# Kernel optimization log

Hardware: AMD Instinct MI355X
Metric: run time of the kernel (lower is better)

## Reference

```python
import jax, jax.numpy as jnp
import numpy as np

EMB = 300; H = 150; DEC = 300
VU = 50000; VQ = 30000; VS = 5000
N_COLS = 64; COL_LEN = 6; N_TURNS = 6; IN_LEN = 128; GEN_LEN = 64
MAX_KEEP = 5


def _lstm_cell(x, h, c, Wih, Whh, b):
    z = x @ Wih.T + h @ Whh.T + b
    i, f, g, o = jnp.split(z, 4)
    c = jax.nn.sigmoid(f) * c + jax.nn.sigmoid(i) * jnp.tanh(g)
    h = jax.nn.sigmoid(o) * jnp.tanh(c)
    return h, c


def _run_lstm(xs, Wih, Whh, b):
    hsz = Whh.shape[-1]
    z = jnp.zeros((hsz,), xs.dtype)
    def step(carry, x):
        h, c = _lstm_cell(x, carry[0], carry[1], Wih, Whh, b)
        return (h, c), h
    (h, c), ys = jax.lax.scan(step, (z, z), xs)
    return ys, h, c


def _bilstm(xs, Wih, Whh, b):
    # Wih: [2, 4H, in], Whh: [2, 4H, H], b: [2, 4H]
    yf, hf, cf = _run_lstm(xs, Wih[0], Whh[0], b[0])
    yb, hb, cb = _run_lstm(xs[::-1], Wih[1], Whh[1], b[1])
    return jnp.concatenate([yf, yb[::-1]], -1), jnp.concatenate([hf, hb], -1), jnp.concatenate([cf, cb], -1)


def _attention(q, keys, Wq, Wk, v):
    # Bahdanau: v^T tanh(Wq q + Wk k); context = softmax-weighted sum of keys
    s = jnp.tanh(q @ Wq + keys @ Wk) @ v
    return jax.nn.softmax(s) @ keys


def _forward(utter_emb, query_emb, schema_tok_emb, enc_Wih, enc_Whh, enc_b,
             attn_Wq, attn_Wk, attn_v, dec_Wih0, dec_Whh0, dec_b0,
             dec_Wih1, dec_Whh1, dec_b1, transform_W, sql_W, sql_b, col_W,
             schema_tokens, input_seqs, output_gt):
    attn = lambda k_i, q, keys: _attention(q, keys, attn_Wq[k_i], attn_Wk[k_i], attn_v[k_i])
    # --- schema column encoding: BiLSTM over each column's name tokens ---
    col_tok = schema_tok_emb[schema_tokens]                       # [C, L, EMB]
    _, h, _ = jax.vmap(lambda xs: _bilstm(xs, enc_Wih[0], enc_Whh[0], enc_b[0]))(col_tok)
    schema_embs = h                                               # [C, EMB]
    prev_in, prev_h, prev_c, prev_out = [], [], [], []
    all_dists = []
    bos_emb = query_emb[0]
    for i in range(N_TURNS):
        idx = input_seqs[i]
        # mixed vocab / schema-pointer embedding lookup
        x = jnp.where((idx < VU)[:, None],
                      utter_emb[jnp.clip(idx, 0, VU - 1)],
                      schema_embs[jnp.clip(idx - VU, 0, N_COLS - 1)])
        x, _, _ = _bilstm(x, enc_Wih[1], enc_Whh[1], enc_b[1])    # utter_encoder
        # TextSchemaEncoder (approx): second BiLSTM + schema cross-attention update
        x, fh, fc = _bilstm(x, enc_Wih[2], enc_Whh[2], enc_b[2])
        schema_embs = schema_embs + jax.nn.softmax(schema_embs @ x.T, -1) @ x
        h0, c0 = fh, fc
        if i > 0:
            hist_h = jnp.stack(prev_h); hist_c = jnp.stack(prev_c)
            h0n = h0 + attn(0, h0, hist_h)
            c0 = h0n + attn(0, c0, hist_c)  # replicates original's h-based c init
            h0 = h0n
        prev_in = (prev_in + [x])[:MAX_KEEP]
        prev_h = (prev_h + [fh])[:MAX_KEEP]
        prev_c = (prev_c + [fc])[:MAX_KEEP]
        keys_in = jnp.concatenate(prev_in, 0)
        keys_out = jnp.concatenate(prev_out, 0) if i > 0 else None
        se = schema_embs

        def embed_out(t):
            return jnp.where(t < VQ,
                             query_emb[jnp.clip(t, 0, VQ - 1)],
                             se[jnp.clip(t - VQ, 0, N_COLS - 1)])

        def dec_step(carry, t):
            h1p, c1p, h2p, c2p, dh = carry
            out_emb = embed_out(t)  # teacher forcing
            ctx_s = attn(1, dh, se)
            ctx_i = attn(2, dh, keys_in)
            ctx_o = attn(3, dh, keys_out) if keys_out is not None else jnp.zeros_like(ctx_i)
            ctx = jnp.concatenate([ctx_s, ctx_i, ctx_o])
            xin = jnp.concatenate([out_emb, ctx])                 # [4*EMB]
            h1, c1 = _lstm_cell(xin, h1p, c1p, dec_Wih0, dec_Whh0, dec_b0)
            h2, c2 = _lstm_cell(h1, h2p, c2p, dec_Wih1, dec_Whh1, dec_b1)
            out = jnp.tanh(jnp.concatenate([h2, ctx]) @ transform_W.T)
            score = jnp.concatenate([out @ sql_W.T + sql_b, (out @ col_W.T) @ se.T])
            dist = jax.nn.log_softmax(score)
            am_emb = embed_out(jnp.argmax(dist))
            return (h1, c1, h2, c2, h2), (dist, am_emb)

        init = (h0, c0, h0, c0, h0)
        _, (dists, am_embs) = jax.lax.scan(dec_step, init, output_gt[i, :GEN_LEN - 1])
        prev_out = (prev_out + [jnp.concatenate([bos_emb[None], am_embs], 0)])[:MAX_KEEP]
        all_dists.append(dists)
    return jnp.stack(all_dists, 0)  # [N_TURNS, GEN_LEN-1, VQ+N_COLS]


def setup_inputs() -> dict:
    key = jax.random.key(0)
    ks = jax.random.split(key, 24)
    s = 0.05
    f = lambda k, shape: jax.random.normal(k, shape, jnp.float32) * s
    return {
        "utter_emb": f(ks[0], (VU, EMB)),
        "query_emb": f(ks[1], (VQ, EMB)),
        "schema_tok_emb": f(ks[2], (VS, EMB)),
        "enc_Wih": f(ks[3], (3, 2, 4 * H, EMB)),   # [schema, utter, text-schema] x [fwd, bwd]
        "enc_Whh": f(ks[4], (3, 2, 4 * H, H)),
        "enc_b": f(ks[5], (3, 2, 4 * H)),
        "attn_Wq": f(ks[6], (4, EMB, EMB)),        # [turn, schema, in_tok, out_tok]
        "attn_Wk": f(ks[7], (4, EMB, EMB)),
        "attn_v": f(ks[8], (4, EMB)),
        "dec_Wih0": f(ks[9], (4 * DEC, 4 * EMB)),
        "dec_Whh0": f(ks[10], (4 * DEC, DEC)),
        "dec_b0": f(ks[11], (4 * DEC,)),
        "dec_Wih1": f(ks[12], (4 * DEC, DEC)),
        "dec_Whh1": f(ks[13], (4 * DEC, DEC)),
        "dec_b1": f(ks[14], (4 * DEC,)),
        "transform_W": f(ks[15], (EMB, 4 * EMB)),
        "sql_W": f(ks[16], (VQ, EMB)),
        "sql_b": f(ks[17], (VQ,)),
        "col_W": f(ks[18], (EMB, EMB)),
        "schema_tokens": jax.random.randint(ks[19], (N_COLS, COL_LEN), 0, VS),
        "input_seqs": jax.random.randint(ks[20], (N_TURNS, IN_LEN), 0, VU + N_COLS),
        "output_gt": jax.random.randint(ks[21], (N_TURNS, GEN_LEN), 0, VQ + N_COLS),
    }


def reference(utter_emb, query_emb, schema_tok_emb, enc_Wih, enc_Whh, enc_b,
              attn_Wq, attn_Wk, attn_v, dec_Wih0, dec_Whh0, dec_b0,
              dec_Wih1, dec_Whh1, dec_b1, transform_W, sql_W, sql_b, col_W,
              schema_tokens, input_seqs, output_gt):
    return _forward(utter_emb, query_emb, schema_tok_emb, enc_Wih, enc_Whh, enc_b,
                    attn_Wq, attn_Wk, attn_v, dec_Wih0, dec_Whh0, dec_b0,
                    dec_Wih1, dec_Whh1, dec_b1, transform_W, sql_W, sql_b, col_W,
                    schema_tokens, input_seqs, output_gt)
```

## Files before the change

kernel.cpp:

```cpp
#include <hip/hip_runtime.h>

#define EMB 300
#define VU 50000
#define VQ 30000
#define NCOLS 64
#define COLLEN 6
#define NTURNS 6
#define INLEN 128
#define TSTEPS 63
#define VOUT 30064
#define MAXK 5
#define NWD 60
#define FPAD 32
#define SENTU 0x7FC00001u

__device__ __forceinline__ float sigf(float x){ return 1.0f/(1.0f+__expf(-x)); }
__device__ __forceinline__ float tanhf_(float x){ return 1.0f - 2.0f/(1.0f+__expf(2.0f*x)); }
__device__ __forceinline__ float wsum(float v){
#pragma unroll
  for (int o=32;o;o>>=1) v += __shfl_xor(v,o);
  return v;
}
__device__ __forceinline__ float wmax(float v){
#pragma unroll
  for (int o=32;o;o>>=1) v = fmaxf(v,__shfl_xor(v,o));
  return v;
}

__device__ __forceinline__ void gstore(float* p, float v){
  __hip_atomic_store((int*)p, __float_as_int(v), __ATOMIC_RELAXED, __HIP_MEMORY_SCOPE_AGENT);
}
__device__ __forceinline__ float gload(const float* p){
  return __int_as_float(__hip_atomic_load((const int*)p, __ATOMIC_RELAXED, __HIP_MEMORY_SCOPE_AGENT));
}

__device__ __forceinline__ void garrive(int* flags, int w, int P){
  asm volatile("s_waitcnt vmcnt(0)" ::: "memory");
  __syncthreads();
  if (threadIdx.x == 0)
    __hip_atomic_store(flags + w*FPAD, P, __ATOMIC_RELAXED, __HIP_MEMORY_SCOPE_AGENT);
}
__device__ __forceinline__ void gwait(const int* flags, int P){
  if (threadIdx.x < 64) {
    int v;
    do {
      v = (threadIdx.x < NWD) ? __hip_atomic_load(flags + threadIdx.x*FPAD, __ATOMIC_RELAXED, __HIP_MEMORY_SCOPE_AGENT) : P;
    } while (__any(v < P));
  }
  __syncthreads();
}

template<int MAXV>
__device__ __forceinline__ void pollfetch(const float* __restrict__ src, float* dstLDS,
                                          int n, int modstride, int tid, volatile int* okf)
{
  float v[MAXV]; bool val[MAXV]; int idx[MAXV];
#pragma unroll
  for (int k = 0; k < MAXV; ++k) {
    idx[k] = tid + 256*k;
    bool ib = idx[k] < n;
    if (modstride) {
      int m = idx[k];
      while (m >= modstride) m -= modstride;
      ib = ib && (m < 300);
    }
    val[k] = ib;
  }
  for (;;) {
    bool ok = true;
#pragma unroll
    for (int k = 0; k < MAXV; ++k)
      if (val[k]) { v[k] = gload(src + idx[k]); ok = ok && (__float_as_uint(v[k]) != SENTU); }
    if (!__all(ok) && (tid & 63) == 0) *okf = 0;
    __syncthreads();
    int done = *okf;
    __syncthreads();
    if (done) break;
    if (tid == 0) *okf = 1;
    __syncthreads();
  }
#pragma unroll
  for (int k = 0; k < MAXV; ++k) if (val[k]) dstLDS[idx[k]] = v[k];
  __syncthreads();
}

__global__ void k_init(int* flags){
  for (int i = threadIdx.x; i < NWD*FPAD; i += 256) flags[i] = 0;
}

__global__ void k_transposeB(const float* __restrict__ in, float* __restrict__ out,
                             int R, int C, size_t mstride)
{
  __shared__ float tile[32][33];
  const float* inp = in + (size_t)blockIdx.z*mstride;
  float* outp = out + (size_t)blockIdx.z*mstride;
  const int rb = blockIdx.y*32, cb = blockIdx.x*32;
  const int tx = threadIdx.x & 31, ty = threadIdx.x >> 5;
  for (int k = 0; k < 32; k += 8) {
    int r = rb + ty + k, c = cb + tx;
    if (r < R && c < C) tile[ty+k][tx] = inp[(size_t)r*C + c];
  }
  __syncthreads();
  for (int k = 0; k < 32; k += 8) {
    int c = cb + ty + k, r = rb + tx;
    if (c < C && r < R) outp[(size_t)c*R + r] = tile[tx][ty+k];
  }
}

__global__ void k_schema(const float* __restrict__ temb, const int* __restrict__ stok,
                         const float* __restrict__ Wih, const float* __restrict__ Whh,
                         const float* __restrict__ bb, float* __restrict__ SE0)
{
  const int col = blockIdx.x >> 1, dir = blockIdx.x & 1, tid = threadIdx.x;
  __shared__ float hl[150], cl[150], zl[600];
  if (tid < 150) { hl[tid]=0.f; cl[tid]=0.f; }
  __syncthreads();
  const float* Wi = Wih + (size_t)dir*600*300;
  const float* Wh = Whh + (size_t)dir*600*150;
  const float* bd = bb + dir*600;
  for (int s = 0; s < COLLEN; ++s) {
    const int pos = dir ? (COLLEN-1-s) : s;
    const int tok = stok[col*COLLEN + pos];
    const float* x = temb + (size_t)tok*300;
    for (int g = tid; g < 600; g += 256) {
      float a = bd[g];
      const float* wi = Wi + (size_t)g*300;
      for (int c = 0; c < 300; ++c) a += x[c]*wi[c];
      const float* wh = Wh + (size_t)g*150;
      for (int j = 0; j < 150; ++j) a += hl[j]*wh[j];
      zl[g] = a;
    }
    __syncthreads();
    if (tid < 150) {
      float ii=zl[tid], ff=zl[150+tid], gg=zl[300+tid], oo=zl[450+tid];
      float cn = sigf(ff)*cl[tid] + sigf(ii)*tanhf_(gg);
      cl[tid]=cn; hl[tid]=sigf(oo)*tanhf_(cn);
    }
    __syncthreads();
  }
  if (tid < 150) SE0[(size_t)col*300 + dir*150 + tid] = hl[tid];
}

__global__ void k_gemm_xe(const float* __restrict__ src, const float* __restrict__ SEi,
                          const int* __restrict__ iseq, int mode,
                          const float* __restrict__ WihT, const float* __restrict__ bL,
                          float* __restrict__ Xg)
{
  const int g = blockIdx.x*256 + threadIdx.x;
  if (g >= 1200) return;
  const int p0 = blockIdx.y*16;
  const float* xr[16];
#pragma unroll
  for (int t = 0; t < 16; ++t) {
    int p = p0 + t;
    if (mode) xr[t] = src + (size_t)p*300;
    else {
      int tok = iseq[p];
      xr[t] = (tok < VU) ? src + (size_t)tok*300 : SEi + (size_t)(tok - VU)*300;
    }
  }
  const float b = bL[g];
  float acc[16];
#pragma unroll
  for (int t = 0; t < 16; ++t) acc[t] = b;
  for (int c = 0; c < 300; ++c) {
    float wv = WihT[(size_t)c*1200 + g];
#pragma unroll
    for (int t = 0; t < 16; ++t) acc[t] += wv * xr[t][c];
  }
#pragma unroll
  for (int t = 0; t < 16; ++t) Xg[(size_t)(p0+t)*1200 + g] = acc[t];
}

__global__ __launch_bounds__(640) void k_rec(
    const float* __restrict__ Xg, const float* __restrict__ WhhTL,
    float* __restrict__ ys, float* __restrict__ fh, float* __restrict__ fc)
{
  const int dir = blockIdx.x, tid = threadIdx.x;
  __shared__ __align__(16) float hl[152];
  __shared__ float cl[152], zl[600];
  float w[150];
  const float* wt = WhhTL + (size_t)dir*150*600;
  if (tid < 600) {
#pragma unroll
    for (int j = 0; j < 150; ++j) w[j] = wt[(size_t)j*600 + tid];
  }
  if (tid < 152) { hl[tid] = 0.f; cl[tid] = 0.f; }
  __syncthreads();
  float xg = (tid < 600) ? Xg[(size_t)(dir ? INLEN-1 : 0)*1200 + dir*600 + tid] : 0.f;
  for (int s = 0; s < INLEN; ++s) {
    const int pos = dir ? (INLEN-1-s) : s;
    const int nxt = dir ? (INLEN-2-s) : (s+1);
    float xg_nx = (s+1 < INLEN && tid < 600) ? Xg[(size_t)nxt*1200 + dir*600 + tid] : 0.f;
    if (tid < 600) {
      float aa[8];
#pragma unroll
      for (int q = 0; q < 8; ++q) aa[q] = 0.f;
      const float4* h4 = (const float4*)hl;
#pragma unroll
      for (int j4 = 0; j4 < 37; ++j4) {
        float4 h = h4[j4];
        aa[j4&7] += w[4*j4]*h.x + w[4*j4+1]*h.y + w[4*j4+2]*h.z + w[4*j4+3]*h.w;
      }
      zl[tid] = xg + ((aa[0]+aa[1])+(aa[2]+aa[3])) + ((aa[4]+aa[5])+(aa[6]+aa[7]))
                + w[148]*hl[148] + w[149]*hl[149];
    }
    __syncthreads();
    if (tid < 150) {
      float ii=zl[tid], ff=zl[150+tid], gg=zl[300+tid], oo=zl[450+tid];
      float cn = sigf(ff)*cl[tid] + sigf(ii)*tanhf_(gg);
      cl[tid] = cn;
      float hn = sigf(oo)*tanhf_(cn);
      hl[tid] = hn;
      ys[(size_t)pos*300 + dir*150 + tid] = hn;
    }
    __syncthreads();
    xg = xg_nx;
  }
  if (tid < 150) { fh[dir*150 + tid] = hl[tid]; fc[dir*150 + tid] = cl[tid]; }
}

__global__ void k_schema_upd(const float* __restrict__ SEi, const float* __restrict__ ys2,
                             float* __restrict__ SEo,
                             const float* __restrict__ fh, const float* __restrict__ fc,
                             float* __restrict__ HH, float* __restrict__ CH,
                             float* __restrict__ XH, int turn)
{
  const int row = blockIdx.x, tid = threadIdx.x;
  __shared__ float sl[300], al[128], red[4];
  for (int d = tid; d < 300; d += 256) sl[d] = SEi[(size_t)row*300 + d];
  __syncthreads();
  if (tid < 128) {
    float a = 0;
    const float* yr = ys2 + (size_t)tid*300;
    for (int d = 0; d < 300; ++d) a += sl[d]*yr[d];
    al[tid] = a;
  }
  __syncthreads();
  if (tid < 64) { float m = fmaxf(al[tid], al[tid+64]); m = wmax(m); if (tid==0) red[0]=m; }
  __syncthreads();
  if (tid < 128) al[tid] = __expf(al[tid] - red[0]);
  __syncthreads();
  if (tid < 64) { float s = al[tid] + al[tid+64]; s = wsum(s); if (tid==0) red[1]=s; }
  __syncthreads();
  const float invz = 1.0f/red[1];
  for (int d = tid; d < 300; d += 256) {
    float a = sl[d];
    for (int j = 0; j < 128; ++j) a += (al[j]*invz) * ys2[(size_t)j*300 + d];
    SEo[(size_t)row*300 + d] = a;
  }
  if (turn < MAXK) {
    for (int i = row*600 + tid; i < row*600 + 600; i += 256)
      XH[(size_t)turn*INLEN*300 + i] = ys2[i];
    if (row == 0)
      for (int d = tid; d < 300; d += 256) { HH[turn*300+d] = fh[d]; CH[turn*300+d] = fc[d]; }
  }
}

__device__ __forceinline__ const float* key_ptr(int j, int nin, const float* SE1,
                                                const float* XH, const float* OH, int* fam)
{
  if (j < 64) { *fam = 0; return SE1 + (size_t)j*300; }
  if (j < 64+nin) { *fam = 1; return XH + (size_t)(j-64)*300; }
  *fam = 2; return OH + (size_t)(j-64-nin)*300;
}

__global__ __launch_bounds__(256) void k_g1k(
    const float* __restrict__ SE1, const float* __restrict__ XH,
    const float* __restrict__ OH, const float* __restrict__ Wih0,
    float* __restrict__ G1KT, int nin, int nout)
{
  const int NK = 64 + nin + nout;
  const int tid = threadIdx.x;
  const int j0 = blockIdx.x*32, r0 = blockIdx.y*64;
  __shared__ float A[32][301];
  int fam; const float* base = key_ptr(j0, nin, SE1, XH, OH, &fam);
  const int wv = tid >> 6, ln = tid & 63;
  for (int jj = wv*8; jj < wv*8+8; ++jj)
    for (int c = ln; c < 300; c += 64)
      A[jj][c] = base[(size_t)jj*300 + c];
  __syncthreads();
  const int j = tid & 31, rb = tid >> 5;
  const int cb = 300 + fam*300;
  float acc[8] = {0,0,0,0,0,0,0,0};
  const float* Wp[8]; bool vld[8];
#pragma unroll
  for (int i = 0; i < 8; ++i) {
    int r = r0 + rb + 8*i;
    vld[i] = (r < 1200);
    Wp[i] = Wih0 + (size_t)(vld[i] ? r : 0)*1200 + cb;
  }
  for (int c = 0; c < 300; ++c) {
    float a = A[j][c];
#pragma unroll
    for (int i = 0; i < 8; ++i) acc[i] += a * Wp[i][c];
  }
#pragma unroll
  for (int i = 0; i < 8; ++i) {
    int r = r0 + rb + 8*i;
    if (vld[i]) G1KT[(size_t)r*NK + j0 + j] = acc[i];
  }
}

__global__ void k_tables(const float* __restrict__ SE1, const float* __restrict__ XH,
                         const float* __restrict__ OH, const float* __restrict__ Wk,
                         const float* __restrict__ Wih0T, const float* __restrict__ b0,
                         const float* __restrict__ tWT, const float* __restrict__ qemb,
                         const int* __restrict__ gt,
                         float* __restrict__ KW, float* __restrict__ G2K,
                         float* __restrict__ Ew, int nin, int nout)
{
  const int NK = 64 + nin + nout;
  const int b = blockIdx.x;
  if (b < NK) {
    int fam; const float* Kr = key_ptr(b, nin, SE1, XH, OH, &fam);
    const float* W = Wk + (size_t)(1+fam)*90000;
    for (int c = threadIdx.x; c < 300; c += 256) {
      float a = 0;
      for (int d = 0; d < 300; ++d) a += Kr[d]*W[(size_t)d*300 + c];
      KW[(size_t)b*300 + c] = a;
    }
  } else if (b < 2*NK) {
    int j = b - NK;
    int fam; const float* Kr = key_ptr(j, nin, SE1, XH, OH, &fam);
    const int cb = 300 + fam*300;
    for (int r = threadIdx.x; r < 300; r += 256) {
      float a = 0;
      for (int c = 0; c < 300; ++c) a += Kr[c]*tWT[(size_t)(cb+c)*300 + r];
      G2K[(size_t)j*300 + r] = a;
    }
  } else {
    int t = b - 2*NK;
    int tok = gt[t];
    const float* e = (tok < VQ) ? qemb + (size_t)tok*300 : SE1 + (size_t)(tok-VQ)*300;
    for (int r = threadIdx.x; r < 1200; r += 256) {
      float a = b0[r];
      for (int c = 0; c < 300; ++c) a += e[c]*Wih0T[(size_t)c*1200 + r];
      Ew[(size_t)t*1200 + r] = a;
    }
  }
}

__global__ __launch_bounds__(256, 1) void k_dec(
    const float* __restrict__ KW, const float* __restrict__ G1KT,
    const float* __restrict__ Ew, const float* __restrict__ WqT,
    const float* __restrict__ av, const float* __restrict__ Wq0,
    const float* __restrict__ Wk0,
    const float* __restrict__ Whh0, const float* __restrict__ Wih1,
    const float* __restrict__ Whh1, const float* __restrict__ b1,
    const float* __restrict__ fh, const float* __restrict__ fc,
    const float* __restrict__ HH, const float* __restrict__ CH,
    float* __restrict__ h0b, float* __restrict__ c0b,
    float* __restrict__ xQW, float* __restrict__ xSC,
    float* __restrict__ xH1, float* __restrict__ xH2,
    float* __restrict__ Alog, float* __restrict__ H2log,
    int nin, int nout, int turn, int* __restrict__ flags)
{
  const int NK = 64 + nin + nout;
  const int w = blockIdx.x, tid = threadIdx.x;
  const int wv = tid >> 6, ln = tid & 63;
  __shared__ float g1kl[20][1024];
  __shared__ float kwl[18][320];
  __shared__ float qWlp[3][320];
  __shared__ float vllp[3][320];
  __shared__ float ewl[63][20];
  __shared__ float scl[1024];
  __shared__ float dhl[320], h1l[320];
  __shared__ float pre1[20], pre2[20], zl[20], c1l[5], c2l[5];
  __shared__ float redA[4], alscA[8];
  __shared__ float wr0[4], wr1[4], wr2[4], rm[3], rz[3];
  __shared__ int okf;
  const float SENTF = __uint_as_float(SENTU);

  for (int i = w*256 + tid; i < TSTEPS*960;  i += NWD*256) gstore(xQW + i, SENTF);
  for (int i = w*256 + tid; i < TSTEPS*1024; i += NWD*256) gstore(xSC + i, SENTF);
  for (int i = w*256 + tid; i < TSTEPS*320;  i += NWD*256) gstore(xH1 + i, SENTF);
  for (int i = w*256 + tid; i < TSTEPS*320;  i += NWD*256) gstore(xH2 + i, SENTF);

  for (int i = tid; i < 20*1024; i += 256) {
    int o = i >> 10, j = i & 1023;
    int row = w*5 + (o % 5) + 300*(o / 5);
    g1kl[o][j] = (j < NK) ? G1KT[(size_t)row*NK + j] : 0.f;
  }
  for (int i = tid; i < 18*320; i += 256) {
    int jo = i / 320, c = i - jo*320;
    int j = w*18 + jo;
    kwl[jo][c] = (c < 300 && j < NK) ? KW[(size_t)j*300 + c] : 0.f;
  }
  for (int i = tid; i < 3*320; i += 256) {
    int f = i / 320, c = i - f*320;
    vllp[f][c] = (c < 300) ? av[300 + f*300 + c] : 0.f;
    qWlp[f][c] = 0.f;
  }
  for (int i = tid; i < 63*20; i += 256) {
    int t = i / 20, o = i - t*20;
    int row = w*5 + (o % 5) + 300*(o / 5);
    ewl[t][o] = Ew[(size_t)t*1200 + row];
  }
  if (tid < 20) { dhl[300+tid] = 0.f; h1l[300+tid] = 0.f; }
  if (tid == 0) okf = 1;

  float rwh0[5][5], rwh1[5][5], rwi1[5][5], rwq4[4][5], b1r[5];
#pragma unroll
  for (int r = 0; r < 5; ++r) {
    int row = w*5 + r + 300*wv;
    b1r[r] = b1[row];
#pragma unroll
    for (int k = 0; k < 5; ++k) {
      int d = ln + 64*k;
      rwh0[r][k] = (d < 300) ? Whh0[(size_t)row*300 + d] : 0.f;
      rwh1[r][k] = (d < 300) ? Whh1[(size_t)row*300 + d] : 0.f;
      rwi1[r][k] = (d < 300) ? Wih1[(size_t)row*300 + d] : 0.f;
    }
  }
#pragma unroll
  for (int r = 0; r < 4; ++r) {
    int o = r*4 + wv;
    int q = w*15 + ((o < 15) ? o : 0);
    int fam = q / 300, c = q - fam*300;
    const float* bp = WqT + ((size_t)(1+fam)*300 + c)*300;
#pragma unroll
    for (int k = 0; k < 5; ++k) {
      int d = ln + 64*k;
      rwq4[r][k] = (o < 15 && d < 300) ? bp[d] : 0.f;
    }
  }
  const int jlo = (w*18 < NK) ? w*18 : NK-1;
  const int jhi = (w*18+17 < NK) ? w*18+17 : NK-1;
  const int f0 = (jlo < 64) ? 0 : (jlo < 64+nin ? 1 : 2);
  const int f1 = (jhi < 64) ? 0 : (jhi < 64+nin ? 1 : 2);
  __syncthreads();

  if (w == 0) {
    if (turn == 0) {
      for (int d = tid; d < 300; d += 256) { gstore(h0b+d, fh[d]); gstore(c0b+d, fc[d]); }
    } else {
      const int nh = turn;
      for (int d = tid; d < 300; d += 256) dhl[d] = fh[d];
      __syncthreads();
      for (int rep = 0; rep < 2; ++rep) {
        const float* keys = rep ? CH : HH;
        for (int c = tid; c < 300; c += 256) {
          float a = 0;
          for (int d = 0; d < 300; ++d) a += dhl[d]*Wq0[(size_t)d*300 + c];
          h1l[c] = a;
        }
        __syncthreads();
        for (int k = 0; k < nh; ++k) {
          const float* Kr = keys + (size_t)k*300;
          float part = 0;
          for (int c = tid; c < 300; c += 256) {
            float kw = 0;
            for (int d = 0; d < 300; ++d) kw += Kr[d]*Wk0[(size_t)d*300 + c];
            part += av[c]*tanhf_(h1l[c] + kw);
          }
          part = wsum(part);
          if (ln == 0) redA[wv] = part;
          __syncthreads();
          if (tid == 0) alscA[k] = redA[0]+redA[1]+redA[2]+redA[3];
          __syncthreads();
        }
        if (tid == 0) {
          float m = -1e30f;
          for (int k = 0; k < nh; ++k) m = fmaxf(m, alscA[k]);
          float z = 0;
          for (int k = 0; k < nh; ++k) { alscA[k] = __expf(alscA[k]-m); z += alscA[k]; }
          for (int k = 0; k < nh; ++k) alscA[k] /= z;
        }
        __syncthreads();
        if (rep == 0) {
          for (int c = tid; c < 300; c += 256) {
            float a = dhl[c];
            for (int k = 0; k < nh; ++k) a += alscA[k]*keys[(size_t)k*300 + c];
            scl[c] = a; gstore(h0b+c, a);
          }
          __syncthreads();
          for (int d = tid; d < 300; d += 256) dhl[d] = fc[d];
          __syncthreads();
        } else {
          for (int c = tid; c < 300; c += 256) {
            float a = scl[c];
            for (int k = 0; k < nh; ++k) a += alscA[k]*keys[(size_t)k*300 + c];
            gstore(c0b+c, a);
          }
        }
      }
    }
  }
  garrive(flags, w, turn+1);
  gwait(flags, turn+1);

  for (int i = tid; i < 300; i += 256) { float v = gload(h0b+i); dhl[i] = v; h1l[i] = v; }
  if (tid < 5) { float v = gload(c0b + w*5 + tid); c1l[tid] = v; c2l[tid] = v; }
  __syncthreads();

  for (int t = 0; t < TSTEPS; ++t) {
    if (t) pollfetch<2>(xH2 + (size_t)(t-1)*320, dhl, 300, 0, tid, &okf);
#pragma unroll
    for (int r = 0; r < 4; ++r) {
      float a = 0;
#pragma unroll
      for (int k = 0; k < 5; ++k) a += rwq4[r][k]*dhl[ln + 64*k];
      a = wsum(a);
      int o = r*4 + wv;
      if (ln == 0 && o < 15) {
        int q = w*15 + o, fam = q/300, c = q - fam*300;
        gstore(xQW + (size_t)t*960 + fam*320 + c, a);
      }
    }
#pragma unroll
    for (int r = 0; r < 5; ++r) {
      float a1 = 0, a2 = 0;
#pragma unroll
      for (int k = 0; k < 5; ++k) {
        float hv = h1l[ln + 64*k], dv = dhl[ln + 64*k];
        a1 += rwh0[r][k]*hv; a2 += rwh1[r][k]*dv;
      }
      a1 = wsum(a1); a2 = wsum(a2);
      if (ln == 0) { pre1[wv*5+r] = a1; pre2[wv*5+r] = a2 + b1r[r]; }
    }

    pollfetch<3>(xQW + (size_t)t*960 + f0*320, &qWlp[f0][0], (f1-f0+1)*320, 320, tid, &okf);
#pragma unroll
    for (int r = 0; r < 5; ++r) {
      int jo = wv*5 + r;
      int j = w*18 + jo;
      bool va = (jo < 18) && (j < NK);
      int f = va ? ((j < 64) ? 0 : (j < 64+nin ? 1 : 2)) : 0;
      int jc = (jo < 18) ? jo : 0;
      float a = 0;
#pragma unroll
      for (int k = 0; k < 5; ++k) {
        int c = ln + 64*k;
        a += vllp[f][c] * tanhf_(qWlp[f][c] + kwl[jc][c]);
      }
      a = wsum(a);
      if (ln == 0 && va) gstore(xSC + (size_t)t*1024 + j, a);
    }

    pollfetch<4>(xSC + (size_t)t*1024, scl, NK, 0, tid, &okf);
    {
      float m0=-1e30f, m1=-1e30f, m2=-1e30f;
      for (int j = tid; j < NK; j += 256) {
        float x = scl[j];
        if (j < 64) m0 = fmaxf(m0,x); else if (j < 64+nin) m1 = fmaxf(m1,x); else m2 = fmaxf(m2,x);
      }
      m0 = wmax(m0); m1 = wmax(m1); m2 = wmax(m2);
      if (ln==0){ wr0[wv]=m0; wr1[wv]=m1; wr2[wv]=m2; }
      __syncthreads();
      if (tid==0){
        rm[0]=fmaxf(fmaxf(wr0[0],wr0[1]),fmaxf(wr0[2],wr0[3]));
        rm[1]=fmaxf(fmaxf(wr1[0],wr1[1]),fmaxf(wr1[2],wr1[3]));
        rm[2]=fmaxf(fmaxf(wr2[0],wr2[1]),fmaxf(wr2[2],wr2[3]));
      }
      __syncthreads();
      float s0=0,s1=0,s2=0;
      for (int j = tid; j < NK; j += 256) {
        int f = (j<64)?0:(j<64+nin?1:2);
        float e = __expf(scl[j] - rm[f]);
        scl[j] = e;
        if (f==0) s0+=e; else if (f==1) s1+=e; else s2+=e;
      }
      s0=wsum(s0); s1=wsum(s1); s2=wsum(s2);
      if (ln==0){ wr0[wv]=s0; wr1[wv]=s1; wr2[wv]=s2; }
      __syncthreads();
      if (tid==0){
        rz[0]=wr0[0]+wr0[1]+wr0[2]+wr0[3];
        rz[1]=wr1[0]+wr1[1]+wr1[2]+wr1[3];
        rz[2]=wr2[0]+wr2[1]+wr2[2]+wr2[3];
      }
      __syncthreads();
      for (int j = tid; j < NK; j += 256) {
        int f = (j<64)?0:(j<64+nin?1:2);
        scl[j] /= rz[f];
      }
      __syncthreads();
    }
    {
      const int KC = NK >> 6;
#pragma unroll 1
      for (int r = 0; r < 5; ++r) {
        int o = wv*5 + r;
        float a = 0;
        for (int k = 0; k < KC; ++k) { int j = ln + 64*k; a += scl[j]*g1kl[o][j]; }
        a = wsum(a);
        if (ln == 0) zl[o] = a + ewl[t][o] + pre1[o];
      }
    }
    __syncthreads();
    if (tid < 5) {
      float ii=zl[tid], ff=zl[5+tid], gg=zl[10+tid], oo=zl[15+tid];
      float cn = sigf(ff)*c1l[tid] + sigf(ii)*tanhf_(gg);
      c1l[tid] = cn;
      gstore(xH1 + (size_t)t*320 + w*5 + tid, sigf(oo)*tanhf_(cn));
    }
    if (tid < 18) { int j = w*18 + tid; if (j < NK) Alog[(size_t)t*1024 + j] = scl[j]; }

    pollfetch<2>(xH1 + (size_t)t*320, h1l, 300, 0, tid, &okf);
#pragma unroll
    for (int r = 0; r < 5; ++r) {
      float a = 0;
#pragma unroll
      for (int k = 0; k < 5; ++k) a += rwi1[r][k]*h1l[ln + 64*k];
      a = wsum(a);
      if (ln == 0) zl[wv*5+r] = a + pre2[wv*5+r];
    }
    __syncthreads();
    if (tid < 5) {
      int d = w*5 + tid;
      float ii=zl[tid], ff=zl[5+tid], gg=zl[10+tid], oo=zl[15+tid];
      float cn = sigf(ff)*c2l[tid] + sigf(ii)*tanhf_(gg);
      c2l[tid] = cn;
      float hn = sigf(oo)*tanhf_(cn);
      gstore(xH2 + (size_t)t*320 + d, hn);
      H2log[(size_t)t*300 + d] = hn;
    }
  }
}

__global__ void k_ctxout2(const float* __restrict__ H2, const float* __restrict__ Al,
                          const float* __restrict__ G2K, const float* __restrict__ tWT,
                          const float* __restrict__ colW,
                          float* __restrict__ o63, float* __restrict__ t63, int NK)
{
  const int t = blockIdx.x, tid = threadIdx.x;
  __shared__ float ol[304], h2l[304];
  for (int d = tid; d < 300; d += 256) h2l[d] = H2[(size_t)t*300 + d];
  __syncthreads();
  for (int r = tid; r < 300; r += 256) {
    float a = 0;
    for (int d = 0; d < 300; ++d) a += h2l[d]*tWT[(size_t)d*300 + r];
    for (int j = 0; j < NK; ++j) a += Al[(size_t)t*1024 + j]*G2K[(size_t)j*300 + r];
    float v = tanhf_(a);
    ol[r] = v;
    o63[(size_t)t*300 + r] = v;
  }
  __syncthreads();
  for (int e = tid; e < 300; e += 256) {
    float a = 0;
    const float* wc = colW + (size_t)e*300;
    for (int d = 0; d < 300; ++d) a += ol[d]*wc[d];
    t63[(size_t)t*300 + e] = a;
  }
}

__global__ void k_score(const float* __restrict__ o63, const float* __restrict__ t63,
                        const float* __restrict__ sqlW, const float* __restrict__ sqlb,
                        const float* __restrict__ SE1, float* __restrict__ Dout)
{
  const int v = blockIdx.x*256 + threadIdx.x;
  if (v >= VOUT) return;
  const int t0 = blockIdx.y*16;
  const int tn = (t0 + 16 <= 63) ? 16 : (63 - t0);
  float acc[16];
#pragma unroll
  for (int k = 0; k < 16; ++k) acc[k] = 0.f;
  if (v < VQ) {
    const float* w = sqlW + (size_t)v*300;
    for (int d = 0; d < 300; ++d) {
      float wv_ = w[d];
#pragma unroll
      for (int k = 0; k < 16; ++k) acc[k] += wv_ * o63[(size_t)(t0+k)*300 + d];
    }
    float b = sqlb[v];
    for (int k = 0; k < tn; ++k) Dout[(size_t)(t0+k)*VOUT + v] = acc[k] + b;
  } else {
    const float* w = SE1 + (size_t)(v - VQ)*300;
    for (int d = 0; d < 300; ++d) {
      float wv_ = w[d];
#pragma unroll
      for (int k = 0; k < 16; ++k) acc[k] += wv_ * t63[(size_t)(t0+k)*300 + d];
    }
    for (int k = 0; k < tn; ++k) Dout[(size_t)(t0+k)*VOUT + v] = acc[k];
  }
}

__global__ void k_lsm(float* __restrict__ rows, const float* __restrict__ qemb,
                      const float* __restrict__ SE1, float* __restrict__ OHt)
{
  const int t = blockIdx.x, tid = threadIdx.x, wv = tid>>6, ln = tid&63;
  float* row = rows + (size_t)t*VOUT;
  __shared__ float rv[4], rs[4];
  __shared__ int ri[4];
  float m = -1e30f; int mi = VOUT;
  for (int j = tid; j < VOUT; j += 256) {
    float x = row[j];
    if (x > m) { m = x; mi = j; }
  }
#pragma unroll
  for (int o = 32; o; o >>= 1) {
    float om = __shfl_xor(m, o); int oi = __shfl_xor(mi, o);
    if (om > m || (om == m && oi < mi)) { m = om; mi = oi; }
  }
  if (ln == 0) { rv[wv] = m; ri[wv] = mi; }
  __syncthreads();
  if (tid == 0) {
    for (int k = 1; k < 4; ++k)
      if (rv[k] > rv[0] || (rv[k] == rv[0] && ri[k] < ri[0])) { rv[0]=rv[k]; ri[0]=ri[k]; }
  }
  __syncthreads();
  const float M = rv[0];
  float s = 0;
  for (int j = tid; j < VOUT; j += 256) s += __expf(row[j] - M);
  s = wsum(s);
  if (ln == 0) rs[wv] = s;
  __syncthreads();
  const float L = M + logf(rs[0]+rs[1]+rs[2]+rs[3]);
  for (int j = tid; j < VOUT; j += 256) row[j] -= L;
  if (OHt) {
    int id = ri[0];
    const float* src = (id < VQ) ? qemb + (size_t)id*300 : SE1 + (size_t)(id-VQ)*300;
    for (int d = tid; d < 300; d += 256) {
      OHt[(size_t)(t+1)*300 + d] = src[d];
      if (t == 0) OHt[d] = qemb[d];
    }
  }
}

extern "C" void kernel_launch(void* const* d_in, const int* in_sizes, int n_in,
                              void* d_out, int out_size, void* d_ws, size_t ws_size,
                              hipStream_t stream)
{
  const float* utter = (const float*)d_in[0];
  const float* qemb  = (const float*)d_in[1];
  const float* temb  = (const float*)d_in[2];
  const float* eWih  = (const float*)d_in[3];
  const float* eWhh  = (const float*)d_in[4];
  const float* eb    = (const float*)d_in[5];
  const float* aWq   = (const float*)d_in[6];
  const float* aWk   = (const float*)d_in[7];
  const float* av    = (const float*)d_in[8];
  const float* dWih0 = (const float*)d_in[9];
  const float* dWhh0 = (const float*)d_in[10];
  const float* db0   = (const float*)d_in[11];
  const float* dWih1 = (const float*)d_in[12];
  const float* dWhh1 = (const float*)d_in[13];
  const float* db1   = (const float*)d_in[14];
  const float* tW    = (const float*)d_in[15];
  const float* sqlW  = (const float*)d_in[16];
  const float* sqlb  = (const float*)d_in[17];
  const float* colW  = (const float*)d_in[18];
  const int* stok    = (const int*)d_in[19];
  const int* iseq    = (const int*)d_in[20];
  const int* ogt     = (const int*)d_in[21];
  float* dout = (float*)d_out;

  float* base = (float*)d_ws;
  size_t off = 0;
  auto A = [&](size_t n)->float*{ float* r = base + off; off += (n + 63) & ~(size_t)63; return r; };
  float* SE    = A(7*64*300);
  float* XH    = A(5*128*300);
  float* OH    = A(5*64*300);
  float* HH    = A(5*300);
  float* CH    = A(5*300);
  float* ys1   = A(128*300);
  float* ys2   = A(128*300);
  float* Xg    = A(128*1200);
  float* fh    = A(320);
  float* fc    = A(320);
  float* fhs   = A(320);
  float* fcs   = A(320);
  float* h0b   = A(320);
  float* c0b   = A(320);
  float* xQW   = A(TSTEPS*960);
  float* xSC   = A(TSTEPS*1024);
  float* xH1   = A(TSTEPS*320);
  float* xH2   = A(TSTEPS*320);
  float* KW    = A(1024*300);
  float* G1KT  = A(1200*1024);
  float* G2K   = A(1024*300);
  float* EwB   = A(63*1200);
  float* Alog  = A(63*1024);
  float* H2lg  = A(64*300);
  float* o63   = A(64*300);
  float* t63   = A(64*300);
  A(512);
  float* WqT   = A(4*300*300);
  float* WhhT  = A(6*150*600);
  float* Wih0T = A(1200*1200);
  float* tWT   = A(1200*300);
  float* eWT   = A(2*300*1200);
  int* flags = (int*)A(NWD*FPAD);
  (void)ws_size; (void)in_sizes; (void)n_in; (void)out_size;

  dim3 B256(256);
  k_init<<<1, B256, 0, stream>>>(flags);
  k_transposeB<<<dim3(10,10,4), B256, 0, stream>>>(aWq, WqT, 300, 300, 90000);
  k_transposeB<<<dim3(5,19,6), B256, 0, stream>>>(eWhh, WhhT, 600, 150, 90000);
  k_transposeB<<<dim3(38,38,1), B256, 0, stream>>>(dWih0, Wih0T, 1200, 1200, 0);
  k_transposeB<<<dim3(38,10,1), B256, 0, stream>>>(tW, tWT, 300, 1200, 0);
  k_transposeB<<<dim3(10,38,2), B256, 0, stream>>>(eWih + 360000, eWT, 1200, 300, 360000);
  k_schema<<<128, B256, 0, stream>>>(temb, stok, eWih, eWhh, eb, SE);

  for (int i = 0; i < NTURNS; ++i) {
    const int kin  = (i+1 < MAXK) ? (i+1) : MAXK;
    const int kout = (i < MAXK) ? i : MAXK;
    const int nin = kin*128, nout = kout*64;
    const int NK = 64 + nin + nout;
    float* SEi = SE + (size_t)i*19200;
    float* SEo = SE + (size_t)(i+1)*19200;

    k_gemm_xe<<<dim3(5,8), B256, 0, stream>>>(utter, SEi, iseq + i*INLEN, 0,
                                              eWT, eb + 1200, Xg);
    k_rec<<<2, 640, 0, stream>>>(Xg, WhhT + 180000, ys1, fhs, fcs);
    k_gemm_xe<<<dim3(5,8), B256, 0, stream>>>(ys1, SEi, iseq + i*INLEN, 1,
                                              eWT + 360000, eb + 2400, Xg);
    k_rec<<<2, 640, 0, stream>>>(Xg, WhhT + 360000, ys2, fh, fc);
    k_schema_upd<<<64, B256, 0, stream>>>(SEi, ys2, SEo, fh, fc, HH, CH, XH, i);
    k_tables<<<2*NK + 63, B256, 0, stream>>>(SEo, XH, OH, aWk, Wih0T, db0, tWT, qemb,
                                             ogt + i*64, KW, G2K, EwB, nin, nout);
    k_g1k<<<dim3(NK/32, 19), B256, 0, stream>>>(SEo, XH, OH, dWih0, G1KT, nin, nout);
    k_dec<<<NWD, B256, 0, stream>>>(KW, G1KT, EwB, WqT, av, aWq, aWk,
                                    dWhh0, dWih1, dWhh1, db1, fh, fc, HH, CH,
                                    h0b, c0b, xQW, xSC, xH1, xH2, Alog, H2lg,
                                    nin, nout, i, flags);
    k_ctxout2<<<63, B256, 0, stream>>>(H2lg, Alog, G2K, tWT, colW, o63, t63, NK);
    k_score<<<dim3(118,4), B256, 0, stream>>>(o63, t63, sqlW, sqlb, SEo, dout + (size_t)i*63*VOUT);
    k_lsm<<<63, B256, 0, stream>>>(dout + (size_t)i*63*VOUT, qemb, SEo,
                                   (i < MAXK) ? OH + (size_t)i*19200 : nullptr);
  }
}
```

Baseline: 18.91 ms.

## Merge table kernels with key tiling, lighten poll barriers, fold softmax normalization

Merges the k_tables and k_g1k kernels into one launch. The KW and G2K products are now computed over 32-key tiles staged in shared memory, so each weight load is reused across 32 keys, and the Ew projection is batched 16 tokens per thread. In the decoder, the cross-device poll loop now exits on a per-wave vote plus s_sleep instead of three block barriers per iteration. The softmax divide pass and its barrier are replaced by per-family reciprocals applied inside the gate reduction and the Alog write. Risks include higher register pressure from the 32-wide accumulators and waves in a block leaving the poll loop at different times.

```diff
diff --git a/kernel.cpp b/kernel.cpp
--- a/kernel.cpp
+++ b/kernel.cpp
@@ -52,7 +52,7 @@
 
 template<int MAXV>
 __device__ __forceinline__ void pollfetch(const float* __restrict__ src, float* dstLDS,
-                                          int n, int modstride, int tid, volatile int* okf)
+                                          int n, int modstride, int tid)
 {
   float v[MAXV]; bool val[MAXV]; int idx[MAXV];
 #pragma unroll
@@ -71,13 +71,8 @@
 #pragma unroll
     for (int k = 0; k < MAXV; ++k)
       if (val[k]) { v[k] = gload(src + idx[k]); ok = ok && (__float_as_uint(v[k]) != SENTU); }
-    if (!__all(ok) && (tid & 63) == 0) *okf = 0;
-    __syncthreads();
-    int done = *okf;
-    __syncthreads();
-    if (done) break;
-    if (tid == 0) *okf = 1;
-    __syncthreads();
+    if (__all(ok)) break;
+    __builtin_amdgcn_s_sleep(1);
   }
 #pragma unroll
   for (int k = 0; k < MAXV; ++k) if (val[k]) dstLDS[idx[k]] = v[k];
@@ -265,78 +260,119 @@
   *fam = 2; return OH + (size_t)(j-64-nin)*300;
 }
 
-__global__ __launch_bounds__(256) void k_g1k(
+__global__ __launch_bounds__(256) void k_tables(
     const float* __restrict__ SE1, const float* __restrict__ XH,
-    const float* __restrict__ OH, const float* __restrict__ Wih0,
-    float* __restrict__ G1KT, int nin, int nout)
+    const float* __restrict__ OH, const float* __restrict__ Wk,
+    const float* __restrict__ Wih0T, const float* __restrict__ b0,
+    const float* __restrict__ tWT, const float* __restrict__ qemb,
+    const int* __restrict__ gt, const float* __restrict__ Wih0,
+    float* __restrict__ KW, float* __restrict__ G2K,
+    float* __restrict__ Ew, float* __restrict__ G1KT,
+    int nin, int nout)
 {
   const int NK = 64 + nin + nout;
+  const int NT32 = NK >> 5;
   const int tid = threadIdx.x;
-  const int j0 = blockIdx.x*32, r0 = blockIdx.y*64;
+  const int b = blockIdx.x;
   __shared__ float A[32][301];
-  int fam; const float* base = key_ptr(j0, nin, SE1, XH, OH, &fam);
-  const int wv = tid >> 6, ln = tid & 63;
-  for (int jj = wv*8; jj < wv*8+8; ++jj)
-    for (int c = ln; c < 300; c += 64)
-      A[jj][c] = base[(size_t)jj*300 + c];
-  __syncthreads();
-  const int j = tid & 31, rb = tid >> 5;
-  const int cb = 300 + fam*300;
-  float acc[8] = {0,0,0,0,0,0,0,0};
-  const float* Wp[8]; bool vld[8];
-#pragma unroll
-  for (int i = 0; i < 8; ++i) {
-    int r = r0 + rb + 8*i;
-    vld[i] = (r < 1200);
-    Wp[i] = Wih0 + (size_t)(vld[i] ? r : 0)*1200 + cb;
-  }
-  for (int c = 0; c < 300; ++c) {
-    float a = A[j][c];
-#pragma unroll
-    for (int i = 0; i < 8; ++i) acc[i] += a * Wp[i][c];
-  }
-#pragma unroll
-  for (int i = 0; i < 8; ++i) {
-    int r = r0 + rb + 8*i;
-    if (vld[i]) G1KT[(size_t)r*NK + j0 + j] = acc[i];
-  }
-}
-
-__global__ void k_tables(const float* __restrict__ SE1, const float* __restrict__ XH,
-                         const float* __restrict__ OH, const float* __restrict__ Wk,
-                         const float* __restrict__ Wih0T, const float* __restrict__ b0,
-                         const float* __restrict__ tWT, const float* __restrict__ qemb,
-                         const int* __restrict__ gt,
-                         float* __restrict__ KW, float* __restrict__ G2K,
-                         float* __restrict__ Ew, int nin, int nout)
-{
-  const int NK = 64 + nin + nout;
-  const int b = blockIdx.x;
-  if (b < NK) {
-    int fam; const float* Kr = key_ptr(b, nin, SE1, XH, OH, &fam);
-    const float* W = Wk + (size_t)(1+fam)*90000;
-    for (int c = threadIdx.x; c < 300; c += 256) {
-      float a = 0;
-      for (int d = 0; d < 300; ++d) a += Kr[d]*W[(size_t)d*300 + c];
-      KW[(size_t)b*300 + c] = a;
-    }
-  } else if (b < 2*NK) {
-    int j = b - NK;
-    int fam; const float* Kr = key_ptr(j, nin, SE1, XH, OH, &fam);
+  const int wv4 = tid >> 6, ln = tid & 63;
+
+  if (b < 2*NT32) {
+    const int j0 = (b < NT32 ? b : b - NT32) * 32;
+    int fam; const float* base = key_ptr(j0, nin, SE1, XH, OH, &fam);
+    for (int jj = wv4*8; jj < wv4*8+8; ++jj)
+      for (int c = ln; c < 300; c += 64)
+        A[jj][c] = base[(size_t)jj*300 + c];
+    __syncthreads();
+    if (b < NT32) {
+      const float* W = Wk + (size_t)(1+fam)*90000;
+      for (int rep = 0; rep < 2; ++rep) {
+        int c = tid + rep*256;
+        if (c < 300) {
+          float acc[32];
+#pragma unroll
+          for (int j = 0; j < 32; ++j) acc[j] = 0.f;
+          for (int d = 0; d < 300; ++d) {
+            float wvv = W[(size_t)d*300 + c];
+#pragma unroll
+            for (int j = 0; j < 32; ++j) acc[j] += A[j][d]*wvv;
+          }
+#pragma unroll
+          for (int j = 0; j < 32; ++j) KW[(size_t)(j0+j)*300 + c] = acc[j];
+        }
+      }
+    } else {
+      const int cb = 300 + fam*300;
+      for (int rep = 0; rep < 2; ++rep) {
+        int r = tid + rep*256;
+        if (r < 300) {
+          float acc[32];
+#pragma unroll
+          for (int j = 0; j < 32; ++j) acc[j] = 0.f;
+          for (int d = 0; d < 300; ++d) {
+            float wvv = tWT[(size_t)(cb+d)*300 + r];
+#pragma unroll
+            for (int j = 0; j < 32; ++j) acc[j] += A[j][d]*wvv;
+          }
+#pragma unroll
+          for (int j = 0; j < 32; ++j) G2K[(size_t)(j0+j)*300 + r] = acc[j];
+        }
+      }
+    }
+  } else if (b < 2*NT32 + 20) {
+    const int idx = b - 2*NT32;
+    const int gx = idx % 5, ty = idx / 5;
+    const int g = gx*256 + tid;
+    const int tb = ty*16;
+    const float* e[16]; bool tv[16];
+#pragma unroll
+    for (int k = 0; k < 16; ++k) {
+      int t = tb + k;
+      tv[k] = (t < 63);
+      int tok = tv[k] ? gt[t] : 0;
+      e[k] = (tok < VQ) ? qemb + (size_t)tok*300 : SE1 + (size_t)(tok-VQ)*300;
+    }
+    if (g < 1200) {
+      float bb = b0[g];
+      float acc[16];
+#pragma unroll
+      for (int k = 0; k < 16; ++k) acc[k] = bb;
+      for (int c = 0; c < 300; ++c) {
+        float wvv = Wih0T[(size_t)c*1200 + g];
+#pragma unroll
+        for (int k = 0; k < 16; ++k) acc[k] += wvv * e[k][c];
+      }
+#pragma unroll
+      for (int k = 0; k < 16; ++k)
+        if (tv[k]) Ew[(size_t)(tb+k)*1200 + g] = acc[k];
+    }
+  } else {
+    const int idx = b - (2*NT32 + 20);
+    const int j0 = (idx % NT32)*32, r0 = (idx / NT32)*64;
+    int fam; const float* base = key_ptr(j0, nin, SE1, XH, OH, &fam);
+    for (int jj = wv4*8; jj < wv4*8+8; ++jj)
+      for (int c = ln; c < 300; c += 64)
+        A[jj][c] = base[(size_t)jj*300 + c];
+    __syncthreads();
+    const int j = tid & 31, rb = tid >> 5;
     const int cb = 300 + fam*300;
-    for (int r = threadIdx.x; r < 300; r += 256) {
-      float a = 0;
-      for (int c = 0; c < 300; ++c) a += Kr[c]*tWT[(size_t)(cb+c)*300 + r];
-      G2K[(size_t)j*300 + r] = a;
-    }
-  } else {
-    int t = b - 2*NK;
-    int tok = gt[t];
-    const float* e = (tok < VQ) ? qemb + (size_t)tok*300 : SE1 + (size_t)(tok-VQ)*300;
-    for (int r = threadIdx.x; r < 1200; r += 256) {
-      float a = b0[r];
-      for (int c = 0; c < 300; ++c) a += e[c]*Wih0T[(size_t)c*1200 + r];
-      Ew[(size_t)t*1200 + r] = a;
+    float acc[8] = {0,0,0,0,0,0,0,0};
+    const float* Wp[8]; bool vld[8];
+#pragma unroll
+    for (int i = 0; i < 8; ++i) {
+      int r = r0 + rb + 8*i;
+      vld[i] = (r < 1200);
+      Wp[i] = Wih0 + (size_t)(vld[i] ? r : 0)*1200 + cb;
+    }
+    for (int c = 0; c < 300; ++c) {
+      float a = A[j][c];
+#pragma unroll
+      for (int i = 0; i < 8; ++i) acc[i] += a * Wp[i][c];
+    }
+#pragma unroll
+    for (int i = 0; i < 8; ++i) {
+      int r = r0 + rb + 8*i;
+      if (vld[i]) G1KT[(size_t)r*NK + j0 + j] = acc[i];
     }
   }
 }
@@ -369,7 +405,6 @@
   __shared__ float pre1[20], pre2[20], zl[20], c1l[5], c2l[5];
   __shared__ float redA[4], alscA[8];
   __shared__ float wr0[4], wr1[4], wr2[4], rm[3], rz[3];
-  __shared__ int okf;
   const float SENTF = __uint_as_float(SENTU);
 
   for (int i = w*256 + tid; i < TSTEPS*960;  i += NWD*256) gstore(xQW + i, SENTF);
@@ -398,7 +433,6 @@
     ewl[t][o] = Ew[(size_t)t*1200 + row];
   }
   if (tid < 20) { dhl[300+tid] = 0.f; h1l[300+tid] = 0.f; }
-  if (tid == 0) okf = 1;
 
   float rwh0[5][5], rwh1[5][5], rwi1[5][5], rwq4[4][5], b1r[5];
 #pragma unroll
@@ -495,7 +529,7 @@
   __syncthreads();
 
   for (int t = 0; t < TSTEPS; ++t) {
-    if (t) pollfetch<2>(xH2 + (size_t)(t-1)*320, dhl, 300, 0, tid, &okf);
+    if (t) pollfetch<2>(xH2 + (size_t)(t-1)*320, dhl, 300, 0, tid);
 #pragma unroll
     for (int r = 0; r < 4; ++r) {
       float a = 0;
@@ -520,7 +554,7 @@
       if (ln == 0) { pre1[wv*5+r] = a1; pre2[wv*5+r] = a2 + b1r[r]; }
     }
 
-    pollfetch<3>(xQW + (size_t)t*960 + f0*320, &qWlp[f0][0], (f1-f0+1)*320, 320, tid, &okf);
+    pollfetch<3>(xQW + (size_t)t*960 + f0*320, &qWlp[f0][0], (f1-f0+1)*320, 320, tid);
 #pragma unroll
     for (int r = 0; r < 5; ++r) {
       int jo = wv*5 + r;
@@ -538,7 +572,7 @@
       if (ln == 0 && va) gstore(xSC + (size_t)t*1024 + j, a);
     }
 
-    pollfetch<4>(xSC + (size_t)t*1024, scl, NK, 0, tid, &okf);
+    pollfetch<4>(xSC + (size_t)t*1024, scl, NK, 0, tid);
     {
       float m0=-1e30f, m1=-1e30f, m2=-1e30f;
       for (int j = tid; j < NK; j += 256) {
@@ -570,19 +604,20 @@
         rz[2]=wr2[0]+wr2[1]+wr2[2]+wr2[3];
       }
       __syncthreads();
-      for (int j = tid; j < NK; j += 256) {
-        int f = (j<64)?0:(j<64+nin?1:2);
-        scl[j] /= rz[f];
-      }
-      __syncthreads();
-    }
+    }
+    const int KC = NK >> 6;
+    const int c1e = 1 + (nin >> 6);
+    float inv0 = 1.0f/rz[0], inv1 = 1.0f/rz[1];
+    float inv2 = (KC > c1e) ? 1.0f/rz[2] : 0.f;
     {
-      const int KC = NK >> 6;
 #pragma unroll 1
       for (int r = 0; r < 5; ++r) {
         int o = wv*5 + r;
-        float a = 0;
-        for (int k = 0; k < KC; ++k) { int j = ln + 64*k; a += scl[j]*g1kl[o][j]; }
+        float a0 = scl[ln]*g1kl[o][ln];
+        float a1 = 0, a2 = 0;
+        for (int k = 1; k < c1e; ++k) { int j = ln + 64*k; a1 += scl[j]*g1kl[o][j]; }
+        for (int k = c1e; k < KC; ++k) { int j = ln + 64*k; a2 += scl[j]*g1kl[o][j]; }
+        float a = a0*inv0 + a1*inv1 + a2*inv2;
         a = wsum(a);
         if (ln == 0) zl[o] = a + ewl[t][o] + pre1[o];
       }
@@ -594,9 +629,16 @@
       c1l[tid] = cn;
       gstore(xH1 + (size_t)t*320 + w*5 + tid, sigf(oo)*tanhf_(cn));
     }
-    if (tid < 18) { int j = w*18 + tid; if (j < NK) Alog[(size_t)t*1024 + j] = scl[j]; }
-
-    pollfetch<2>(xH1 + (size_t)t*320, h1l, 300, 0, tid, &okf);
+    if (tid < 18) {
+      int j = w*18 + tid;
+      if (j < NK) {
+        int f = (j<64)?0:(j<64+nin?1:2);
+        float iv = (f==0)?inv0:((f==1)?inv1:inv2);
+        Alog[(size_t)t*1024 + j] = scl[j]*iv;
+      }
+    }
+
+    pollfetch<2>(xH1 + (size_t)t*320, h1l, 300, 0, tid);
 #pragma unroll
     for (int r = 0; r < 5; ++r) {
       float a = 0;
@@ -797,6 +839,7 @@
     const int kout = (i < MAXK) ? i : MAXK;
     const int nin = kin*128, nout = kout*64;
     const int NK = 64 + nin + nout;
+    const int NT32 = NK/32;
     float* SEi = SE + (size_t)i*19200;
     float* SEo = SE + (size_t)(i+1)*19200;
 
@@ -807,9 +850,9 @@
                                               eWT + 360000, eb + 2400, Xg);
     k_rec<<<2, 640, 0, stream>>>(Xg, WhhT + 360000, ys2, fh, fc);
     k_schema_upd<<<64, B256, 0, stream>>>(SEi, ys2, SEo, fh, fc, HH, CH, XH, i);
-    k_tables<<<2*NK + 63, B256, 0, stream>>>(SEo, XH, OH, aWk, Wih0T, db0, tWT, qemb,
-                                             ogt + i*64, KW, G2K, EwB, nin, nout);
-    k_g1k<<<dim3(NK/32, 19), B256, 0, stream>>>(SEo, XH, OH, dWih0, G1KT, nin, nout);
+    k_tables<<<2*NT32 + 20 + NT32*19, B256, 0, stream>>>(
+        SEo, XH, OH, aWk, Wih0T, db0, tWT, qemb, ogt + i*64, dWih0,
+        KW, G2K, EwB, G1KT, nin, nout);
     k_dec<<<NWD, B256, 0, stream>>>(KW, G1KT, EwB, WqT, av, aWq, aWk,
                                     dWhh0, dWih1, dWhh1, db1, fh, fc, HH, CH,
                                     h0b, c0b, xQW, xSC, xH1, xH2, Alog, H2lg,
```

New measurement: 19.58 ms. 1.04x slower.
